# Optimization experiments

Hardware: AMD Instinct MI355X
Metric: run time of the kernel (lower is better)

## Reference

```python
import jax, jax.numpy as jnp
import numpy as np

NL, NK = 10000, 2000          # ligand / keypoint node counts
ELL, EKL = 320000, 160000     # lig->lig and kp->lig edge counts
IN, HID, OUT = 128, 128, 128  # in_size, hidden_size, out_size
FDIM = 2 * IN + 1             # edge MLP input: [h_src, h_dst, dij]


def silu(x):
    return x * jax.nn.sigmoid(x)


def setup_inputs() -> dict:
    keys = iter(jax.random.split(jax.random.key(0), 64))

    def nrm(shape, scale=0.02):
        return jax.random.normal(next(keys), shape, dtype=jnp.float32) * scale

    d = {}
    d["h_lig"] = jax.random.normal(next(keys), (NL, IN), dtype=jnp.float32)
    d["h_kp"] = jax.random.normal(next(keys), (NK, IN), dtype=jnp.float32)
    d["x_lig"] = jax.random.normal(next(keys), (NL, 3), dtype=jnp.float32)
    d["x_kp"] = jax.random.normal(next(keys), (NK, 3), dtype=jnp.float32)
    # per-node normalizer (e.g. neighbor count); keep >= 1 to avoid blowup
    d["z_lig"] = jax.random.uniform(next(keys), (NL, 1), dtype=jnp.float32, minval=1.0, maxval=32.0)
    for e in ("ll", "kl"):
        d[e + "_eW1"] = nrm((FDIM, HID)); d[e + "_eb1"] = jnp.zeros((HID,), jnp.float32)
        d[e + "_eW2"] = nrm((HID, HID)); d[e + "_eb2"] = jnp.zeros((HID,), jnp.float32)
        d[e + "_aW"] = nrm((HID, 1)); d[e + "_ab"] = jnp.zeros((1,), jnp.float32)
        d[e + "_cW1"] = nrm((FDIM, HID)); d[e + "_cb1"] = jnp.zeros((HID,), jnp.float32)
        d[e + "_cW2"] = nrm((HID, HID)); d[e + "_cb2"] = jnp.zeros((HID,), jnp.float32)
        d[e + "_cW3"] = nrm((HID, 1), scale=0.001)  # xavier gain=0.001 final coord layer
    d["n_W1"] = nrm((IN + HID, HID)); d["n_b1"] = jnp.zeros((HID,), jnp.float32)
    d["n_W2"] = nrm((HID, OUT)); d["n_b2"] = jnp.zeros((OUT,), jnp.float32)
    d["ll_src"] = jax.random.randint(next(keys), (ELL,), 0, NL, dtype=jnp.int32)
    d["ll_dst"] = jax.random.randint(next(keys), (ELL,), 0, NL, dtype=jnp.int32)
    d["kl_src"] = jax.random.randint(next(keys), (EKL,), 0, NK, dtype=jnp.int32)
    d["kl_dst"] = jax.random.randint(next(keys), (EKL,), 0, NL, dtype=jnp.int32)
    return d


def _edge_messages(hs, hd, xs, xd, eW1, eb1, eW2, eb2, aW, ab, cW1, cb1, cW2, cb2, cW3):
    x_diff = xs - xd                                     # fn.u_sub_v
    dij = jnp.linalg.norm(x_diff, axis=1, keepdims=True)  # [E,1]
    x_diff = x_diff / (dij + 1.0)
    f = jnp.concatenate([hs, hd, dij], axis=1)           # [E, 2*IN+1]
    m = silu(f @ eW1 + eb1)
    m = silu(m @ eW2 + eb2)
    msg_h = m * jax.nn.sigmoid(m @ aW + ab)              # soft attention gate
    c = silu(f @ cW1 + cb1)
    c = silu(c @ cW2 + cb2)
    msg_x = (c @ cW3) * x_diff                           # use_tanh=False path
    return msg_h, msg_x


def reference(h_lig, h_kp, x_lig, x_kp, z_lig,
              ll_eW1, ll_eb1, ll_eW2, ll_eb2, ll_aW, ll_ab,
              ll_cW1, ll_cb1, ll_cW2, ll_cb2, ll_cW3,
              kl_eW1, kl_eb1, kl_eW2, kl_eb2, kl_aW, kl_ab,
              kl_cW1, kl_cb1, kl_cW2, kl_cb2, kl_cW3,
              n_W1, n_b1, n_W2, n_b2,
              ll_src, ll_dst, kl_src, kl_dst):
    # lig -> lig edges
    mh_ll, mx_ll = _edge_messages(h_lig[ll_src], h_lig[ll_dst], x_lig[ll_src], x_lig[ll_dst],
                                  ll_eW1, ll_eb1, ll_eW2, ll_eb2, ll_aW, ll_ab,
                                  ll_cW1, ll_cb1, ll_cW2, ll_cb2, ll_cW3)
    # kp -> lig edges
    mh_kl, mx_kl = _edge_messages(h_kp[kl_src], h_lig[kl_dst], x_kp[kl_src], x_lig[kl_dst],
                                  kl_eW1, kl_eb1, kl_eW2, kl_eb2, kl_aW, kl_ab,
                                  kl_cW1, kl_cb1, kl_cW2, kl_cb2, kl_cW3)
    nl = h_lig.shape[0]
    # multi_update_all with cross_reducer='sum', then per-node normalization by z
    h_neigh = (jax.ops.segment_sum(mh_ll, ll_dst, num_segments=nl)
               + jax.ops.segment_sum(mh_kl, kl_dst, num_segments=nl)) / z_lig
    x_neigh = (jax.ops.segment_sum(mx_ll, ll_dst, num_segments=nl)
               + jax.ops.segment_sum(mx_kl, kl_dst, num_segments=nl)) / z_lig
    nin = jnp.concatenate([h_lig, h_neigh], axis=1)
    h_out = h_lig + (silu(nin @ n_W1 + n_b1) @ n_W2 + n_b2)  # norm=False -> Identity
    x_out = x_lig + x_neigh
    return (h_out, x_out)
```

## Files before the change

kernel.cpp:

```cpp
#include <hip/hip_runtime.h>
#include <hip/hip_bf16.h>
#include <math.h>

#define EPB  32
#define MSTR 136
#define FSTR 264

typedef __attribute__((ext_vector_type(8))) short short8;
typedef __attribute__((ext_vector_type(4))) float f32x4;

__device__ __forceinline__ unsigned short f2bf(float x) {
    unsigned int u = __float_as_uint(x);
    u += 0x7fffu + ((u >> 16) & 1u);
    return (unsigned short)(u >> 16);
}
__device__ __forceinline__ float bf2f(short v) {
    return __uint_as_float(((unsigned int)(unsigned short)v) << 16);
}
__device__ __forceinline__ unsigned int pkbf(float a, float b) {
    __hip_bfloat162 h = __float22bfloat162_rn(make_float2(a, b));
    union { __hip_bfloat162 h2; unsigned int u; } cv; cv.h2 = h; return cv.u;
}
__device__ __forceinline__ float frcp(float x) { return __builtin_amdgcn_rcpf(x); }
__device__ __forceinline__ float fsilu(float x) {
    return x * frcp(1.0f + __expf(-x));
}
__device__ __forceinline__ float fsigm(float x) {
    return frcp(1.0f + __expf(-x));
}
__device__ __forceinline__ void atomAddF(float* p, float v) {
    unsafeAtomicAdd(p, v);
}

struct PrepArgs { const float* src[10]; };

__global__ __launch_bounds__(256) void prep_hist_kernel(PrepArgs pa, short* __restrict__ wsb,
                                                        const int* __restrict__ lld,
                                                        const int* __restrict__ kld,
                                                        int* __restrict__ hist) {
    int idx = blockIdx.x * 256 + threadIdx.x;
    if (idx < 245760) {
        int pair = idx / 49152;
        int rem  = idx - pair * 49152;
        int second = (rem >= 32768) ? 1 : 0;
        int mi = pair * 2 + second;
        int within = second ? (rem - 32768) : rem;
        int n, k, K;
        if (second) { K = 128; n = within >> 7; k = within & 127; }
        else        { K = 256; n = within >> 8; k = within & 255; }
        int dstoff = pair * 49152 + second * 32768;
        wsb[dstoff + n * K + k] = (short)f2bf(pa.src[mi][k * 128 + n]);
        return;
    }
    idx -= 245760;
    if (idx < 320000) { atomicAdd(&hist[lld[idx]], 1); return; }
    idx -= 320000;
    if (idx < 160000) atomicAdd(&hist[10000 + kld[idx]], 1);
}

__global__ __launch_bounds__(256) void scan_kernel(const int* __restrict__ hist,
                                                   int* __restrict__ cursor) {
    __shared__ int bins[10000];
    __shared__ int ps[256];
    const int b = blockIdx.x, t = threadIdx.x;
    const int* h = hist + b * 10000;
    int* cur = cursor + b * 10000;
    for (int i = t; i < 10000; i += 256) bins[i] = h[i];
    __syncthreads();
    const int base = t * 40;
    int s = 0;
#pragma unroll 8
    for (int i = 0; i < 40; i++) { int ii = base + i; if (ii < 10000) s += bins[ii]; }
    ps[t] = s;
    __syncthreads();
    for (int off = 1; off < 256; off <<= 1) {
        int v = (t >= off) ? ps[t - off] : 0;
        __syncthreads();
        ps[t] += v;
        __syncthreads();
    }
    int run = ps[t] - s;
    for (int i = 0; i < 40; i++) {
        int ii = base + i;
        if (ii < 10000) { int c = bins[ii]; bins[ii] = run; run += c; }
    }
    __syncthreads();
    for (int i = t; i < 10000; i += 256) cur[i] = bins[i];
}

struct ProjDesc { const float* A; const short* Bt; short* out; const float* bias;
                  int rows; int ktb; int co; int hasb; };
struct CArgs {
    const int *lls, *lld, *kls, *kld;
    int* cursor;
    int *ll_ssrc, *ll_sdst, *kl_ssrc, *kl_sdst;
    ProjDesc d[8];
};

__global__ __launch_bounds__(256) void scatter_proj_kernel(CArgs ca) {
    __shared__ __align__(16) short a_lds[64 * MSTR];
    const int t = threadIdx.x;
    if (blockIdx.x < 1875) {
        int i = blockIdx.x * 256 + t;
        if (i < 320000) {
            int d = ca.lld[i];
            int p = atomicAdd(&ca.cursor[d], 1);
            ca.ll_ssrc[p] = ca.lls[i]; ca.ll_sdst[p] = d;
        } else if (i < 480000) {
            int j = i - 320000;
            int d = ca.kld[j];
            int p = atomicAdd(&ca.cursor[10000 + d], 1);
            ca.kl_ssrc[p] = ca.kls[j]; ca.kl_sdst[p] = d;
        }
        return;
    }
    const int pb = blockIdx.x - 1875;
    const int di = pb / 157, tile = pb - di * 157;
    const ProjDesc pd = ca.d[di];
    if (tile * 64 >= pd.rows) return;
    {
        const int r = t >> 2, q = t & 3;
        const int node = tile * 64 + r;
        short* arow = a_lds + r * MSTR + q * 32;
        if (node < pd.rows) {
            const float* ap = pd.A + (size_t)node * 128 + q * 32;
#pragma unroll
            for (int i = 0; i < 4; i++) {
                float4 v0 = *(const float4*)(ap + i * 8);
                float4 v1 = *(const float4*)(ap + i * 8 + 4);
                uint4 o;
                o.x = pkbf(v0.x, v0.y); o.y = pkbf(v0.z, v0.w);
                o.z = pkbf(v1.x, v1.y); o.w = pkbf(v1.z, v1.w);
                *(uint4*)(arow + i * 8) = o;
            }
        } else {
            uint4 z = make_uint4(0, 0, 0, 0);
#pragma unroll
            for (int i = 0; i < 4; i++) *(uint4*)(arow + i * 8) = z;
        }
    }
    __syncthreads();

    const int ln = t & 63, wv = t >> 6;
    const int lrow = ln & 15, quad = ln >> 4;
    const int c0 = wv * 32 + lrow, c1 = c0 + 16;

    short8 bf0[4], bf1[4];
#pragma unroll
    for (int kt = 0; kt < 4; kt++) {
        bf0[kt] = *(const short8*)(pd.Bt + c0 * 256 + (pd.ktb + kt) * 32 + quad * 8);
        bf1[kt] = *(const short8*)(pd.Bt + c1 * 256 + (pd.ktb + kt) * 32 + quad * 8);
    }
    const float bb0 = pd.hasb ? pd.bias[c0] : 0.0f;
    const float bb1 = pd.hasb ? pd.bias[c1] : 0.0f;
#pragma unroll
    for (int mt = 0; mt < 4; mt++) {
        short8 af[4];
#pragma unroll
        for (int kt = 0; kt < 4; kt++)
            af[kt] = *(const short8*)(&a_lds[(mt * 16 + lrow) * MSTR + kt * 32 + quad * 8]);
        f32x4 a0 = {0.f, 0.f, 0.f, 0.f}, a1 = {0.f, 0.f, 0.f, 0.f};
#pragma unroll
        for (int kt = 0; kt < 4; kt++) {
            a0 = __builtin_amdgcn_mfma_f32_16x16x32_bf16(af[kt], bf0[kt], a0, 0, 0, 0);
            a1 = __builtin_amdgcn_mfma_f32_16x16x32_bf16(af[kt], bf1[kt], a1, 0, 0, 0);
        }
#pragma unroll
        for (int r = 0; r < 4; r++) {
            const int node = tile * 64 + mt * 16 + quad * 4 + r;
            if (node < pd.rows) {
                pd.out[(size_t)node * 256 + pd.co + c0] = (short)f2bf(a0[r] + bb0);
                pd.out[(size_t)node * 256 + pd.co + c1] = (short)f2bf(a1[r] + bb1);
            }
        }
    }
}

struct EdgeSet {
    const short *Ps, *Pd;
    const float *xs, *xd;
    const int *esrc, *edst;
    const float *w256e, *w256c;
    const short *W2t, *cW2t;
    const float *b2e, *b2c;
    const float *aW, *ab, *cW3;
};
struct EdgePair { EdgeSet s[2]; int split; };

__global__ __launch_bounds__(256, 8) void edge_kernel(EdgePair ep,
                                                      float* __restrict__ hne,
                                                      float* __restrict__ xne)
{
    __shared__ __align__(16) char mbuf[EPB * MSTR * 4];
    __shared__ float sv_l[EPB];
    __shared__ float gate_l[EPB];
    __shared__ float xdf[3][EPB];
    __shared__ int   dstl[EPB];
    __shared__ float gpc[4][EPB];
    __shared__ float gpe[4][EPB];

    short* mh = (short*)mbuf;
    short* mc = (short*)(mbuf + EPB * MSTR * 2);
    float* msg = (float*)mbuf;

    const int isKL = (blockIdx.x >= ep.split) ? 1 : 0;
    const EdgeSet P = ep.s[isKL];
    int b = blockIdx.x - (isKL ? ep.split : 0);
    const int nb8 = isKL ? 625 : 1250;
    b = (b & 7) * nb8 + (b >> 3);
    const int eb = b * EPB;
    const int t = threadIdx.x;

    {
        const int e = t >> 3, q = t & 7;
        const int eid = eb + e;
        const int s = P.esrc[eid], d = P.edst[eid];
        float dx = P.xs[s * 3 + 0] - P.xd[d * 3 + 0];
        float dy = P.xs[s * 3 + 1] - P.xd[d * 3 + 1];
        float dz = P.xs[s * 3 + 2] - P.xd[d * 3 + 2];
        float dd = __builtin_amdgcn_sqrtf(dx * dx + dy * dy + dz * dz);
        if (q == 0) {
            dstl[e] = d;
            float inv = frcp(dd + 1.0f);
            xdf[0][e] = dx * inv; xdf[1][e] = dy * inv; xdf[2][e] = dz * inv;
        }
        const short* psrow = P.Ps + (size_t)s * 256 + q * 16;
        const short* pdrow = P.Pd + (size_t)d * 256 + q * 16;
#pragma unroll
        for (int path = 0; path < 2; path++) {
            const short* ps = psrow + path * 128;
            const short* pq = pdrow + path * 128;
            const float* wq = (path ? P.w256c : P.w256e) + q * 16;
            short* mrow = (path ? mc : mh) + e * MSTR + q * 16;
#pragma unroll
            for (int i = 0; i < 2; i++) {
                short8 a = *(const short8*)(ps + i * 8);
                short8 b2 = *(const short8*)(pq + i * 8);
                float4 wA = *(const float4*)(wq + i * 8);
                float4 wB = *(const float4*)(wq + i * 8 + 4);
                float v0 = fsilu(bf2f(a[0]) + bf2f(b2[0]) + dd * wA.x);
                float v1 = fsilu(bf2f(a[1]) + bf2f(b2[1]) + dd * wA.y);
                float v2 = fsilu(bf2f(a[2]) + bf2f(b2[2]) + dd * wA.z);
                float v3 = fsilu(bf2f(a[3]) + bf2f(b2[3]) + dd * wA.w);
                float v4 = fsilu(bf2f(a[4]) + bf2f(b2[4]) + dd * wB.x);
                float v5 = fsilu(bf2f(a[5]) + bf2f(b2[5]) + dd * wB.y);
                float v6 = fsilu(bf2f(a[6]) + bf2f(b2[6]) + dd * wB.z);
                float v7 = fsilu(bf2f(a[7]) + bf2f(b2[7]) + dd * wB.w);
                uint4 o;
                o.x = pkbf(v0, v1); o.y = pkbf(v2, v3);
                o.z = pkbf(v4, v5); o.w = pkbf(v6, v7);
                *(uint4*)(mrow + i * 8) = o;
            }
        }
    }
    __syncthreads();

    const int ln = t & 63, wv = t >> 6;
    const int lrow = ln & 15, quad = ln >> 4;
    const int c0 = wv * 32 + lrow, c1 = c0 + 16;

    {
        short8 bf0[4], bf1[4];
#pragma unroll
        for (int kt = 0; kt < 4; kt++) {
            bf0[kt] = *(const short8*)(P.cW2t + c0 * 128 + kt * 32 + quad * 8);
            bf1[kt] = *(const short8*)(P.cW2t + c1 * 128 + kt * 32 + quad * 8);
        }
        const float cw0 = P.cW3[c0], cw1 = P.cW3[c1];
        const float bb0 = P.b2c[c0], bb1 = P.b2c[c1];
#pragma unroll
        for (int mt = 0; mt < 2; mt++) {
            short8 af[4];
#pragma unroll
            for (int kt = 0; kt < 4; kt++)
                af[kt] = *(const short8*)(&mc[(mt * 16 + lrow) * MSTR + kt * 32 + quad * 8]);
            f32x4 a0 = {0.f, 0.f, 0.f, 0.f}, a1 = {0.f, 0.f, 0.f, 0.f};
#pragma unroll
            for (int kt = 0; kt < 4; kt++) {
                a0 = __builtin_amdgcn_mfma_f32_16x16x32_bf16(af[kt], bf0[kt], a0, 0, 0, 0);
                a1 = __builtin_amdgcn_mfma_f32_16x16x32_bf16(af[kt], bf1[kt], a1, 0, 0, 0);
            }
#pragma unroll
            for (int r = 0; r < 4; r++) {
                float v0 = fsilu(a0[r] + bb0);
                float v1 = fsilu(a1[r] + bb1);
                float g = v0 * cw0 + v1 * cw1;
                g += __shfl_xor(g, 1, 64);
                g += __shfl_xor(g, 2, 64);
                g += __shfl_xor(g, 4, 64);
                g += __shfl_xor(g, 8, 64);
                if (lrow == 0) gpc[wv][mt * 16 + quad * 4 + r] = g;
            }
        }
    }

    float m2s[2][8];
    {
        short8 bf0[4], bf1[4];
#pragma unroll
        for (int kt = 0; kt < 4; kt++) {
            bf0[kt] = *(const short8*)(P.W2t + c0 * 128 + kt * 32 + quad * 8);
            bf1[kt] = *(const short8*)(P.W2t + c1 * 128 + kt * 32 + quad * 8);
        }
        const float aw0 = P.aW[c0], aw1 = P.aW[c1];
        const float bb0 = P.b2e[c0], bb1 = P.b2e[c1];
#pragma unroll
        for (int mt = 0; mt < 2; mt++) {
            short8 af[4];
#pragma unroll
            for (int kt = 0; kt < 4; kt++)
                af[kt] = *(const short8*)(&mh[(mt * 16 + lrow) * MSTR + kt * 32 + quad * 8]);
            f32x4 a0 = {0.f, 0.f, 0.f, 0.f}, a1 = {0.f, 0.f, 0.f, 0.f};
#pragma unroll
            for (int kt = 0; kt < 4; kt++) {
                a0 = __builtin_amdgcn_mfma_f32_16x16x32_bf16(af[kt], bf0[kt], a0, 0, 0, 0);
                a1 = __builtin_amdgcn_mfma_f32_16x16x32_bf16(af[kt], bf1[kt], a1, 0, 0, 0);
            }
#pragma unroll
            for (int r = 0; r < 4; r++) {
                float v0 = fsilu(a0[r] + bb0);
                float v1 = fsilu(a1[r] + bb1);
                m2s[mt][r] = v0; m2s[mt][4 + r] = v1;
                float g = v0 * aw0 + v1 * aw1;
                g += __shfl_xor(g, 1, 64);
                g += __shfl_xor(g, 2, 64);
                g += __shfl_xor(g, 4, 64);
                g += __shfl_xor(g, 8, 64);
                if (lrow == 0) gpe[wv][mt * 16 + quad * 4 + r] = g;
            }
        }
    }
    __syncthreads();

    if (t < EPB) {
        sv_l[t]   = gpc[0][t] + gpc[1][t] + gpc[2][t] + gpc[3][t];
        gate_l[t] = fsigm(gpe[0][t] + gpe[1][t] + gpe[2][t] + gpe[3][t] + P.ab[0]);
    }
#pragma unroll
    for (int mt = 0; mt < 2; mt++)
#pragma unroll
        for (int r = 0; r < 4; r++) {
            const int erow = mt * 16 + quad * 4 + r;
            msg[erow * 132 + c0] = m2s[mt][r];
            msg[erow * 132 + c1] = m2s[mt][4 + r];
        }
    __syncthreads();

    if (t < 128) {
        const int col = t;
        float acc = 0.0f;
        int cur = dstl[0];
#pragma unroll 4
        for (int e = 0; e < EPB; e++) {
            const int d = dstl[e];
            if (d != cur) {
                atomAddF(&hne[(size_t)cur * 128 + col], acc);
                acc = 0.0f; cur = d;
            }
            acc += msg[e * 132 + col] * gate_l[e];
        }
        atomAddF(&hne[(size_t)cur * 128 + col], acc);
    } else if (t < 131) {
        const int ax = t - 128;
        float acc = 0.0f;
        int cur = dstl[0];
        for (int e = 0; e < EPB; e++) {
            const int d = dstl[e];
            if (d != cur) {
                atomAddF(&xne[cur * 3 + ax], acc);
                acc = 0.0f; cur = d;
            }
            acc += sv_l[e] * xdf[ax][e];
        }
        atomAddF(&xne[cur * 3 + ax], acc);
    }
}

__global__ __launch_bounds__(256) void node_kernel(
    const float* __restrict__ h_lig, const float* __restrict__ zlig,
    const short* __restrict__ W1t, const float* __restrict__ b1v,
    const short* __restrict__ W2t, const float* __restrict__ b2v,
    const float* __restrict__ x_lig,
    const float* __restrict__ acc_h, const float* __restrict__ acc_x,
    float* __restrict__ h_out, float* __restrict__ x_out)
{
    __shared__ __align__(16) short f_lds[64 * FSTR];
    __shared__ __align__(16) short m_lds[64 * MSTR];
    const int t = threadIdx.x;
    const int nb = blockIdx.x * 64;

    {
        const int e = t >> 2, q = t & 3;
        const int node = nb + e;
        short* frow = &f_lds[e * FSTR + q * 32];
        if (node < 10000) {
            const float zi = frcp(zlig[node]);
            const float4* hp = (const float4*)(h_lig + (size_t)node * 128 + q * 32);
            const float4* np = (const float4*)(acc_h + (size_t)node * 128 + q * 32);
#pragma unroll
            for (int i = 0; i < 8; i++) {
                float4 v = hp[i];
                *(uint2*)(frow + i * 4) = make_uint2(pkbf(v.x, v.y), pkbf(v.z, v.w));
            }
#pragma unroll
            for (int i = 0; i < 8; i++) {
                float4 v = np[i];
                *(uint2*)(frow + 128 + i * 4) =
                    make_uint2(pkbf(v.x * zi, v.y * zi), pkbf(v.z * zi, v.w * zi));
            }
        } else {
            const uint2 zz = make_uint2(0, 0);
#pragma unroll
            for (int i = 0; i < 8; i++) {
                *(uint2*)(frow + i * 4) = zz;
                *(uint2*)(frow + 128 + i * 4) = zz;
            }
        }
    }
    __syncthreads();

    const int ln = t & 63, wv = t >> 6;
    const int lrow = ln & 15, quad = ln >> 4;
    const int c0 = wv * 32 + lrow, c1 = c0 + 16;

    {
        short8 bf0[8], bf1[8];
#pragma unroll
        for (int kt = 0; kt < 8; kt++) {
            bf0[kt] = *(const short8*)(W1t + c0 * 256 + kt * 32 + quad * 8);
            bf1[kt] = *(const short8*)(W1t + c1 * 256 + kt * 32 + quad * 8);
        }
        const float bb0 = b1v[c0], bb1 = b1v[c1];
#pragma unroll
        for (int mt = 0; mt < 4; mt++) {
            short8 af[8];
#pragma unroll
            for (int kt = 0; kt < 8; kt++)
                af[kt] = *(const short8*)(&f_lds[(mt * 16 + lrow) * FSTR + kt * 32 + quad * 8]);
            f32x4 a0 = {0.f, 0.f, 0.f, 0.f}, a1 = {0.f, 0.f, 0.f, 0.f};
#pragma unroll
            for (int kt = 0; kt < 8; kt++) {
                a0 = __builtin_amdgcn_mfma_f32_16x16x32_bf16(af[kt], bf0[kt], a0, 0, 0, 0);
                a1 = __builtin_amdgcn_mfma_f32_16x16x32_bf16(af[kt], bf1[kt], a1, 0, 0, 0);
            }
#pragma unroll
            for (int r = 0; r < 4; r++) {
                const int erow = mt * 16 + quad * 4 + r;
                m_lds[erow * MSTR + c0] = (short)f2bf(fsilu(a0[r] + bb0));
                m_lds[erow * MSTR + c1] = (short)f2bf(fsilu(a1[r] + bb1));
            }
        }
    }
    __syncthreads();

    {
        short8 bf0[4], bf1[4];
#pragma unroll
        for (int kt = 0; kt < 4; kt++) {
            bf0[kt] = *(const short8*)(W2t + c0 * 128 + kt * 32 + quad * 8);
            bf1[kt] = *(const short8*)(W2t + c1 * 128 + kt * 32 + quad * 8);
        }
        const float bb0 = b2v[c0], bb1 = b2v[c1];
#pragma unroll
        for (int mt = 0; mt < 4; mt++) {
            short8 af[4];
#pragma unroll
            for (int kt = 0; kt < 4; kt++)
                af[kt] = *(const short8*)(&m_lds[(mt * 16 + lrow) * MSTR + kt * 32 + quad * 8]);
            f32x4 a0 = {0.f, 0.f, 0.f, 0.f}, a1 = {0.f, 0.f, 0.f, 0.f};
#pragma unroll
            for (int kt = 0; kt < 4; kt++) {
                a0 = __builtin_amdgcn_mfma_f32_16x16x32_bf16(af[kt], bf0[kt], a0, 0, 0, 0);
                a1 = __builtin_amdgcn_mfma_f32_16x16x32_bf16(af[kt], bf1[kt], a1, 0, 0, 0);
            }
#pragma unroll
            for (int r = 0; r < 4; r++) {
                const int node = nb + mt * 16 + quad * 4 + r;
                if (node < 10000) {
                    h_out[(size_t)node * 128 + c0] = a0[r] + bb0 + h_lig[(size_t)node * 128 + c0];
                    h_out[(size_t)node * 128 + c1] = a1[r] + bb1 + h_lig[(size_t)node * 128 + c1];
                }
            }
        }
    }
    if (t < 64) {
        const int node = nb + t;
        if (node < 10000) {
            const float zi = frcp(zlig[node]);
#pragma unroll
            for (int i = 0; i < 3; i++)
                x_out[node * 3 + i] = x_lig[node * 3 + i] + acc_x[node * 3 + i] * zi;
        }
    }
}

extern "C" void kernel_launch(void* const* d_in, const int* in_sizes, int n_in,
                              void* d_out, int out_size, void* d_ws, size_t ws_size,
                              hipStream_t stream)
{
    (void)in_sizes; (void)n_in; (void)ws_size; (void)out_size;
    const float* h_lig  = (const float*)d_in[0];
    const float* h_kp   = (const float*)d_in[1];
    const float* x_lig  = (const float*)d_in[2];
    const float* x_kp   = (const float*)d_in[3];
    const float* z_lig  = (const float*)d_in[4];
    const float* ll_eW1 = (const float*)d_in[5];
    const float* ll_eb1 = (const float*)d_in[6];
    const float* ll_eW2 = (const float*)d_in[7];
    const float* ll_eb2 = (const float*)d_in[8];
    const float* ll_aW  = (const float*)d_in[9];
    const float* ll_ab  = (const float*)d_in[10];
    const float* ll_cW1 = (const float*)d_in[11];
    const float* ll_cb1 = (const float*)d_in[12];
    const float* ll_cW2 = (const float*)d_in[13];
    const float* ll_cb2 = (const float*)d_in[14];
    const float* ll_cW3 = (const float*)d_in[15];
    const float* kl_eW1 = (const float*)d_in[16];
    const float* kl_eb1 = (const float*)d_in[17];
    const float* kl_eW2 = (const float*)d_in[18];
    const float* kl_eb2 = (const float*)d_in[19];
    const float* kl_aW  = (const float*)d_in[20];
    const float* kl_ab  = (const float*)d_in[21];
    const float* kl_cW1 = (const float*)d_in[22];
    const float* kl_cb1 = (const float*)d_in[23];
    const float* kl_cW2 = (const float*)d_in[24];
    const float* kl_cb2 = (const float*)d_in[25];
    const float* kl_cW3 = (const float*)d_in[26];
    const float* n_W1   = (const float*)d_in[27];
    const float* n_b1   = (const float*)d_in[28];
    const float* n_W2   = (const float*)d_in[29];
    const float* n_b2   = (const float*)d_in[30];
    const int* ll_src = (const int*)d_in[31];
    const int* ll_dst = (const int*)d_in[32];
    const int* kl_src = (const int*)d_in[33];
    const int* kl_dst = (const int*)d_in[34];

    float* h_out = (float*)d_out;
    float* x_out = h_out + 1280000;

    char* wsc = (char*)d_ws;
    short* wsb    = (short*)wsc;
    short* P_ll_s = (short*)(wsc +   491520);
    short* P_ll_d = (short*)(wsc +  5611520);
    short* P_kl_s = (short*)(wsc + 10731520);
    short* P_kl_d = (short*)(wsc + 11755520);
    int* ll_ssrc  = (int*)(wsc + 16875520);
    int* ll_sdst  = (int*)(wsc + 18155520);
    int* kl_ssrc  = (int*)(wsc + 19435520);
    int* kl_sdst  = (int*)(wsc + 20075520);
    int* hist     = (int*)(wsc + 20715520);
    int* cursor   = (int*)(wsc + 20795520);
    float* hne    = (float*)(wsc + 20875520);
    float* xne    = (float*)(wsc + 25995520);

    hipMemsetAsync(hne, 0, 5240000, stream);
    hipMemsetAsync(hist, 0, 80000, stream);

    {
        PrepArgs pa;
        pa.src[0] = ll_eW1; pa.src[1] = ll_eW2; pa.src[2] = ll_cW1; pa.src[3] = ll_cW2;
        pa.src[4] = kl_eW1; pa.src[5] = kl_eW2; pa.src[6] = kl_cW1; pa.src[7] = kl_cW2;
        pa.src[8] = n_W1;   pa.src[9] = n_W2;
        prep_hist_kernel<<<2835, 256, 0, stream>>>(pa, wsb, ll_dst, kl_dst, hist);
    }
    scan_kernel<<<2, 256, 0, stream>>>(hist, cursor);
    {
        CArgs ca;
        ca.lls = ll_src; ca.lld = ll_dst; ca.kls = kl_src; ca.kld = kl_dst;
        ca.cursor = cursor;
        ca.ll_ssrc = ll_ssrc; ca.ll_sdst = ll_sdst;
        ca.kl_ssrc = kl_ssrc; ca.kl_sdst = kl_sdst;
        ca.d[0] = { h_lig, wsb + 0,      P_ll_s, ll_eb1, 10000, 0, 0,   0 };
        ca.d[1] = { h_lig, wsb + 49152,  P_ll_s, ll_cb1, 10000, 0, 128, 0 };
        ca.d[2] = { h_lig, wsb + 0,      P_ll_d, ll_eb1, 10000, 4, 0,   1 };
        ca.d[3] = { h_lig, wsb + 49152,  P_ll_d, ll_cb1, 10000, 4, 128, 1 };
        ca.d[4] = { h_kp,  wsb + 98304,  P_kl_s, kl_eb1,  2000, 0, 0,   0 };
        ca.d[5] = { h_kp,  wsb + 147456, P_kl_s, kl_cb1,  2000, 0, 128, 0 };
        ca.d[6] = { h_lig, wsb + 98304,  P_kl_d, kl_eb1, 10000, 4, 0,   1 };
        ca.d[7] = { h_lig, wsb + 147456, P_kl_d, kl_cb1, 10000, 4, 128, 1 };
        scatter_proj_kernel<<<1875 + 8 * 157, 256, 0, stream>>>(ca);
    }
    {
        EdgePair ep;
        ep.split = 10000;
        ep.s[0] = { P_ll_s, P_ll_d, x_lig, x_lig, ll_ssrc, ll_sdst,
                    ll_eW1 + 256 * 128, ll_cW1 + 256 * 128,
                    wsb + 32768, wsb + 81920, ll_eb2, ll_cb2,
                    ll_aW, ll_ab, ll_cW3 };
        ep.s[1] = { P_kl_s, P_kl_d, x_kp, x_lig, kl_ssrc, kl_sdst,
                    kl_eW1 + 256 * 128, kl_cW1 + 256 * 128,
                    wsb + 131072, wsb + 180224, kl_eb2, kl_cb2,
                    kl_aW, kl_ab, kl_cW3 };
        edge_kernel<<<15000, 256, 0, stream>>>(ep, hne, xne);
    }
    node_kernel<<<157, 256, 0, stream>>>(
        h_lig, z_lig, wsb + 196608, n_b1, wsb + 229376, n_b2,
        x_lig, hne, xne, h_out, x_out);
}
```

Baseline: 399.7 us.

## Pack edge indices, fold zero-fill into prep, use DPP reductions, split scatter

Sorted edge src/dst indices are stored as a packed int2 array so the edge kernel does one 8-byte load per edge instead of two separate loads. The memset of the accumulation buffers is replaced by extra threads in the prep kernel that write float4 zeros, which removes one memset launch. The 16-lane row reductions switch from shfl_xor to DPP row operations. The per-block segmented atomic scatter now uses all 256 threads, each covering half of the edges, instead of 128 threads walking all 32. The split scatter can issue more atomics at node boundaries that cross the halves.

```diff
diff --git a/kernel.cpp b/kernel.cpp
--- a/kernel.cpp
+++ b/kernel.cpp
@@ -32,12 +32,26 @@
     unsafeAtomicAdd(p, v);
 }
 
+template<int CTRL>
+__device__ __forceinline__ float dppAdd(float x) {
+    int y = __builtin_amdgcn_update_dpp(0, __float_as_int(x), CTRL, 0xF, 0xF, false);
+    return x + __int_as_float(y);
+}
+__device__ __forceinline__ float rowSum16(float g) {
+    g = dppAdd<0xB1>(g);
+    g = dppAdd<0x4E>(g);
+    g = dppAdd<0x124>(g);
+    g = dppAdd<0x128>(g);
+    return g;
+}
+
 struct PrepArgs { const float* src[10]; };
 
 __global__ __launch_bounds__(256) void prep_hist_kernel(PrepArgs pa, short* __restrict__ wsb,
                                                         const int* __restrict__ lld,
                                                         const int* __restrict__ kld,
-                                                        int* __restrict__ hist) {
+                                                        int* __restrict__ hist,
+                                                        float* __restrict__ zfill) {
     int idx = blockIdx.x * 256 + threadIdx.x;
     if (idx < 245760) {
         int pair = idx / 49152;
@@ -55,7 +69,10 @@
     idx -= 245760;
     if (idx < 320000) { atomicAdd(&hist[lld[idx]], 1); return; }
     idx -= 320000;
-    if (idx < 160000) atomicAdd(&hist[10000 + kld[idx]], 1);
+    if (idx < 160000) { atomicAdd(&hist[10000 + kld[idx]], 1); return; }
+    idx -= 160000;
+    if (idx < 327500)
+        ((float4*)zfill)[idx] = make_float4(0.f, 0.f, 0.f, 0.f);
 }
 
 __global__ __launch_bounds__(256) void scan_kernel(const int* __restrict__ hist,
@@ -93,7 +110,7 @@
 struct CArgs {
     const int *lls, *lld, *kls, *kld;
     int* cursor;
-    int *ll_ssrc, *ll_sdst, *kl_ssrc, *kl_sdst;
+    int2 *ll_spk, *kl_spk;
     ProjDesc d[8];
 };
 
@@ -103,14 +120,16 @@
     if (blockIdx.x < 1875) {
         int i = blockIdx.x * 256 + t;
         if (i < 320000) {
+            int s = ca.lls[i];
             int d = ca.lld[i];
             int p = atomicAdd(&ca.cursor[d], 1);
-            ca.ll_ssrc[p] = ca.lls[i]; ca.ll_sdst[p] = d;
+            ca.ll_spk[p] = make_int2(s, d);
         } else if (i < 480000) {
             int j = i - 320000;
+            int s = ca.kls[j];
             int d = ca.kld[j];
             int p = atomicAdd(&ca.cursor[10000 + d], 1);
-            ca.kl_ssrc[p] = ca.kls[j]; ca.kl_sdst[p] = d;
+            ca.kl_spk[p] = make_int2(s, d);
         }
         return;
     }
@@ -179,7 +198,7 @@
 struct EdgeSet {
     const short *Ps, *Pd;
     const float *xs, *xd;
-    const int *esrc, *edst;
+    const int2 *esd;
     const float *w256e, *w256c;
     const short *W2t, *cW2t;
     const float *b2e, *b2c;
@@ -214,7 +233,8 @@
     {
         const int e = t >> 3, q = t & 7;
         const int eid = eb + e;
-        const int s = P.esrc[eid], d = P.edst[eid];
+        const int2 sd = P.esd[eid];
+        const int s = sd.x, d = sd.y;
         float dx = P.xs[s * 3 + 0] - P.xd[d * 3 + 0];
         float dy = P.xs[s * 3 + 1] - P.xd[d * 3 + 1];
         float dz = P.xs[s * 3 + 2] - P.xd[d * 3 + 2];
@@ -284,11 +304,7 @@
             for (int r = 0; r < 4; r++) {
                 float v0 = fsilu(a0[r] + bb0);
                 float v1 = fsilu(a1[r] + bb1);
-                float g = v0 * cw0 + v1 * cw1;
-                g += __shfl_xor(g, 1, 64);
-                g += __shfl_xor(g, 2, 64);
-                g += __shfl_xor(g, 4, 64);
-                g += __shfl_xor(g, 8, 64);
+                float g = rowSum16(v0 * cw0 + v1 * cw1);
                 if (lrow == 0) gpc[wv][mt * 16 + quad * 4 + r] = g;
             }
         }
@@ -321,11 +337,7 @@
                 float v0 = fsilu(a0[r] + bb0);
                 float v1 = fsilu(a1[r] + bb1);
                 m2s[mt][r] = v0; m2s[mt][4 + r] = v1;
-                float g = v0 * aw0 + v1 * aw1;
-                g += __shfl_xor(g, 1, 64);
-                g += __shfl_xor(g, 2, 64);
-                g += __shfl_xor(g, 4, 64);
-                g += __shfl_xor(g, 8, 64);
+                float g = rowSum16(v0 * aw0 + v1 * aw1);
                 if (lrow == 0) gpe[wv][mt * 16 + quad * 4 + r] = g;
             }
         }
@@ -346,12 +358,13 @@
         }
     __syncthreads();
 
-    if (t < 128) {
-        const int col = t;
+    {
+        const int col = t & 127;
+        const int e0 = (t >> 7) * 16;
         float acc = 0.0f;
-        int cur = dstl[0];
+        int cur = dstl[e0];
 #pragma unroll 4
-        for (int e = 0; e < EPB; e++) {
+        for (int e = e0; e < e0 + 16; e++) {
             const int d = dstl[e];
             if (d != cur) {
                 atomAddF(&hne[(size_t)cur * 128 + col], acc);
@@ -360,11 +373,13 @@
             acc += msg[e * 132 + col] * gate_l[e];
         }
         atomAddF(&hne[(size_t)cur * 128 + col], acc);
-    } else if (t < 131) {
-        const int ax = t - 128;
+    }
+    if (t < 6) {
+        const int ax = (t >= 3) ? (t - 3) : t;
+        const int e0 = (t >= 3) ? 16 : 0;
         float acc = 0.0f;
-        int cur = dstl[0];
-        for (int e = 0; e < EPB; e++) {
+        int cur = dstl[e0];
+        for (int e = e0; e < e0 + 16; e++) {
             const int d = dstl[e];
             if (d != cur) {
                 atomAddF(&xne[cur * 3 + ax], acc);
@@ -544,16 +559,13 @@
     short* P_ll_d = (short*)(wsc +  5611520);
     short* P_kl_s = (short*)(wsc + 10731520);
     short* P_kl_d = (short*)(wsc + 11755520);
-    int* ll_ssrc  = (int*)(wsc + 16875520);
-    int* ll_sdst  = (int*)(wsc + 18155520);
-    int* kl_ssrc  = (int*)(wsc + 19435520);
-    int* kl_sdst  = (int*)(wsc + 20075520);
+    int2* ll_spk  = (int2*)(wsc + 16875520);
+    int2* kl_spk  = (int2*)(wsc + 19435520);
     int* hist     = (int*)(wsc + 20715520);
     int* cursor   = (int*)(wsc + 20795520);
     float* hne    = (float*)(wsc + 20875520);
     float* xne    = (float*)(wsc + 25995520);
 
-    hipMemsetAsync(hne, 0, 5240000, stream);
     hipMemsetAsync(hist, 0, 80000, stream);
 
     {
@@ -561,15 +573,14 @@
         pa.src[0] = ll_eW1; pa.src[1] = ll_eW2; pa.src[2] = ll_cW1; pa.src[3] = ll_cW2;
         pa.src[4] = kl_eW1; pa.src[5] = kl_eW2; pa.src[6] = kl_cW1; pa.src[7] = kl_cW2;
         pa.src[8] = n_W1;   pa.src[9] = n_W2;
-        prep_hist_kernel<<<2835, 256, 0, stream>>>(pa, wsb, ll_dst, kl_dst, hist);
+        prep_hist_kernel<<<4115, 256, 0, stream>>>(pa, wsb, ll_dst, kl_dst, hist, hne);
     }
     scan_kernel<<<2, 256, 0, stream>>>(hist, cursor);
     {
         CArgs ca;
         ca.lls = ll_src; ca.lld = ll_dst; ca.kls = kl_src; ca.kld = kl_dst;
         ca.cursor = cursor;
-        ca.ll_ssrc = ll_ssrc; ca.ll_sdst = ll_sdst;
-        ca.kl_ssrc = kl_ssrc; ca.kl_sdst = kl_sdst;
+        ca.ll_spk = ll_spk; ca.kl_spk = kl_spk;
         ca.d[0] = { h_lig, wsb + 0,      P_ll_s, ll_eb1, 10000, 0, 0,   0 };
         ca.d[1] = { h_lig, wsb + 49152,  P_ll_s, ll_cb1, 10000, 0, 128, 0 };
         ca.d[2] = { h_lig, wsb + 0,      P_ll_d, ll_eb1, 10000, 4, 0,   1 };
@@ -583,11 +594,11 @@
     {
         EdgePair ep;
         ep.split = 10000;
-        ep.s[0] = { P_ll_s, P_ll_d, x_lig, x_lig, ll_ssrc, ll_sdst,
+        ep.s[0] = { P_ll_s, P_ll_d, x_lig, x_lig, ll_spk,
                     ll_eW1 + 256 * 128, ll_cW1 + 256 * 128,
                     wsb + 32768, wsb + 81920, ll_eb2, ll_cb2,
                     ll_aW, ll_ab, ll_cW3 };
-        ep.s[1] = { P_kl_s, P_kl_d, x_kp, x_lig, kl_ssrc, kl_sdst,
+        ep.s[1] = { P_kl_s, P_kl_d, x_kp, x_lig, kl_spk,
                     kl_eW1 + 256 * 128, kl_cW1 + 256 * 128,
                     wsb + 131072, wsb + 180224, kl_eb2, kl_cb2,
                     kl_aW, kl_ab, kl_cW3 };
```

Measured after the change: 374.5 us. -6.3%, faster.
